# Performance work log

Measured on AMD Instinct MI355X. Metric: run time of the kernel, lower is better.

## Reference

```python
import jax, jax.numpy as jnp
import numpy as np

WS = 7
NHEAD = 8


def setup_inputs() -> dict:
    key = jax.random.key(0)
    k1, k2, k3 = jax.random.split(key, 3)
    B, H, W, D = 32, 56, 56, 256
    x = jax.random.normal(k1, (B, H, W, D), dtype=jnp.float32)
    in_proj_w = jax.random.normal(k2, (3 * D, D), dtype=jnp.float32) * 0.02
    in_proj_b = jnp.zeros((3 * D,), dtype=jnp.float32)
    out_w = jax.random.normal(k3, (D, D), dtype=jnp.float32) * 0.02
    out_b = jnp.zeros((D,), dtype=jnp.float32)
    return {"x": x, "in_proj_w": in_proj_w, "in_proj_b": in_proj_b,
            "out_w": out_w, "out_b": out_b}


def reference(x, in_proj_w, in_proj_b, out_w, out_b):
    B, Hf, Wf, D = x.shape
    ws = WS
    hd = D // NHEAD
    pad_h = (-Hf) % ws
    pad_w = (-Wf) % ws
    xp = jnp.pad(x, ((0, 0), (0, pad_h), (0, pad_w), (0, 0)))
    Hp, Wp = Hf + pad_h, Wf + pad_w
    nh, nw = Hp // ws, Wp // ws
    # partition into windows: [B*nh*nw, ws*ws, D]
    xw = xp.reshape(B, nh, ws, nw, ws, D).transpose(0, 1, 3, 2, 4, 5)
    xw = xw.reshape(B * nh * nw, ws * ws, D)
    N, L = xw.shape[0], ws * ws
    # qkv projection (torch MHA: x @ in_proj_w.T + in_proj_b)
    qkv = jnp.einsum('nld,ed->nle', xw, in_proj_w) + in_proj_b  # [N, L, 3D]
    q, k, v = jnp.split(qkv, 3, axis=-1)
    q = q.reshape(N, L, NHEAD, hd).transpose(0, 2, 1, 3)
    k = k.reshape(N, L, NHEAD, hd).transpose(0, 2, 1, 3)
    v = v.reshape(N, L, NHEAD, hd).transpose(0, 2, 1, 3)
    scale = 1.0 / np.sqrt(hd).astype(np.float32)
    scores = jnp.einsum('nhqd,nhkd->nhqk', q * scale, k)  # [N, H, L, L]
    attn = jax.nn.softmax(scores, axis=-1)
    o = jnp.einsum('nhqk,nhkd->nhqd', attn, v)
    o = o.transpose(0, 2, 1, 3).reshape(N, L, D)
    o = jnp.einsum('nld,ed->nle', o, out_w) + out_b
    # un-window
    o = o.reshape(B, nh, nw, ws, ws, D).transpose(0, 1, 3, 2, 4, 5)
    o = o.reshape(B, Hp, Wp, D)
    return o[:, :Hf, :Wf, :]
```

## Files before the change

### kernel.cpp

```cpp
#include <hip/hip_runtime.h>


using f16   = _Float16;
using f16x4 = __attribute__((ext_vector_type(4))) _Float16;
using f16x8 = __attribute__((ext_vector_type(8))) _Float16;
using f32x4 = __attribute__((ext_vector_type(4))) float;

#define NTOK   100352
#define DMODEL 256
#define QKVN   768
#define QKV_BYTES 154140672ull
#define WQ_HALVES 196608
#define WO_HALVES 65536

typedef const __attribute__((address_space(1))) unsigned int* as1_u32p;
typedef __attribute__((address_space(3))) unsigned int* as3_u32p;

__device__ __forceinline__ void gload16(const void* g, void* l) {
    __builtin_amdgcn_global_load_lds((as1_u32p)g, (as3_u32p)l, 16, 0, 0);
}

__device__ __forceinline__ f16x8 zero8() {
    f16x8 z;
#pragma unroll
    for (int i = 0; i < 8; ++i) z[i] = (f16)0;
    return z;
}

#define XV4   6422528
#define WQV4  49152
#define WOV4  16384
__global__ __launch_bounds__(256) void convert_all(
    const float* __restrict__ X, const float* __restrict__ Wq,
    const float* __restrict__ Wo,
    f16* __restrict__ Xh, f16* __restrict__ Wqh, f16* __restrict__ Woh)
{
    const float scale = 0.17677669529663687f;
    const int total = XV4 + WQV4 + WOV4;
    for (int i = blockIdx.x * blockDim.x + threadIdx.x; i < total;
         i += gridDim.x * blockDim.x) {
        float4 f;
        f16x4 h;
        if (i < XV4) {
            f = reinterpret_cast<const float4*>(X)[i];
            h[0]=(f16)f.x; h[1]=(f16)f.y; h[2]=(f16)f.z; h[3]=(f16)f.w;
            reinterpret_cast<f16x4*>(Xh)[i] = h;
        } else if (i < XV4 + WQV4) {
            int idx = i - XV4;
            int row = idx >> 6;
            float sc = (row < 256) ? scale : 1.0f;
            f = reinterpret_cast<const float4*>(Wq)[idx];
            h[0]=(f16)(f.x*sc); h[1]=(f16)(f.y*sc); h[2]=(f16)(f.z*sc); h[3]=(f16)(f.w*sc);
            reinterpret_cast<f16x4*>(Wqh)[idx] = h;
        } else if (Woh) {
            int idx = i - XV4 - WQV4;
            f = reinterpret_cast<const float4*>(Wo)[idx];
            h[0]=(f16)f.x; h[1]=(f16)f.y; h[2]=(f16)f.z; h[3]=(f16)f.w;
            reinterpret_cast<f16x4*>(Woh)[idx] = h;
        }
    }
}

__global__ __launch_bounds__(256) void qkv_gemm(
    const f16* __restrict__ Xh,
    const f16* __restrict__ Wh,
    const float* __restrict__ bias,
    f16* __restrict__ QKV)
{
    __shared__ f16 As[2][128 * 64];
    __shared__ f16 Bs[2][128 * 64];
    const int tid  = threadIdx.x;
    const int lane = tid & 63;
    const int wave = tid >> 6;
    int wg = blockIdx.x;
    const int cpx = (NTOK / 128) * (QKVN / 128) / 8;
    wg = (wg & 7) * cpx + (wg >> 3);
    const int m0 = (wg / (QKVN / 128)) * 128;
    const int n0 = (wg % (QKVN / 128)) * 128;
    const int wm = (wave >> 1) * 64;
    const int wn = (wave & 1) * 64;
    const int g  = lane >> 4;
    const int lr = lane & 15;

    auto stage = [&](int buf, int k0) {
#pragma unroll
        for (int j = 0; j < 4; ++j) {
            int s   = tid + j * 256;
            int row = s >> 3, sl = s & 7;
            int ss  = sl ^ (row & 7);
            gload16(Xh + (size_t)(m0 + row) * 256 + k0 + ss * 8, &As[buf][s * 8]);
            gload16(Wh + (size_t)(n0 + row) * 256 + k0 + ss * 8, &Bs[buf][s * 8]);
        }
    };

    stage(0, 0);
    __syncthreads();

    f32x4 acc[4][4] = {};
    int buf = 0;
    for (int t = 0; t < 4; ++t) {
        if (t < 3) stage(buf ^ 1, (t + 1) * 64);
#pragma unroll
        for (int ks = 0; ks < 2; ++ks) {
            f16x8 a[4], b[4];
#pragma unroll
            for (int i = 0; i < 4; ++i) {
                int row = wm + i * 16 + lr;
                int c   = ((ks << 2) + g) ^ (row & 7);
                a[i] = *reinterpret_cast<const f16x8*>(&As[buf][row * 64 + c * 8]);
            }
#pragma unroll
            for (int i = 0; i < 4; ++i) {
                int row = wn + i * 16 + lr;
                int c   = ((ks << 2) + g) ^ (row & 7);
                b[i] = *reinterpret_cast<const f16x8*>(&Bs[buf][row * 64 + c * 8]);
            }
#pragma unroll
            for (int mi = 0; mi < 4; ++mi)
#pragma unroll
                for (int ni = 0; ni < 4; ++ni)
                    acc[mi][ni] = __builtin_amdgcn_mfma_f32_16x16x32_f16(a[mi], b[ni], acc[mi][ni], 0, 0, 0);
        }
        __syncthreads();
        buf ^= 1;
    }
    const float scale = 0.17677669529663687f;
#pragma unroll
    for (int ni = 0; ni < 4; ++ni) {
        int n = n0 + wn + ni * 16 + lr;
        float bv = bias[n];
        if (n < 256) bv *= scale;
#pragma unroll
        for (int mi = 0; mi < 4; ++mi)
#pragma unroll
            for (int r = 0; r < 4; ++r) {
                int m = m0 + wm + mi * 16 + g * 4 + r;
                QKV[(size_t)m * QKVN + n] = (f16)(acc[mi][ni][r] + bv);
            }
    }
}

__global__ __launch_bounds__(256) void win_attn(f16* __restrict__ QKV)
{
    __shared__ f16 Vt[4][32][68];
    __shared__ f16 P[4][64][68];
    const int tid  = threadIdx.x;
    const int lane = tid & 63;
    const int w    = tid >> 6;
    const int u    = blockIdx.x * 4 + w;
    const int win = u >> 3, h = u & 7;
    const int b = win >> 6, wh = (win >> 3) & 7, ww = win & 7;
    const int base = (b * 56 + wh * 7) * 56 + ww * 7;
    const int g = lane >> 4, lr = lane & 15;

    auto tok = [&](int row) { int rr = row / 7; return base + rr * 56 + (row - rr * 7); };

    f16x8 qf[4], kf[4];
#pragma unroll
    for (int i = 0; i < 4; ++i) {
        int row = i * 16 + lr;
        if (row < 49) {
            size_t off = (size_t)tok(row) * QKVN + h * 32 + g * 8;
            qf[i] = *reinterpret_cast<const f16x8*>(QKV + off);
            kf[i] = *reinterpret_cast<const f16x8*>(QKV + off + 256);
        } else { qf[i] = zero8(); kf[i] = zero8(); }
    }
    {
        int kk = lane;
        if (kk < 49) {
            size_t off = (size_t)tok(kk) * QKVN + 512 + h * 32;
            f16x8 vv[4];
#pragma unroll
            for (int j = 0; j < 4; ++j)
                vv[j] = *reinterpret_cast<const f16x8*>(QKV + off + j * 8);
#pragma unroll
            for (int j = 0; j < 4; ++j)
#pragma unroll
                for (int d = 0; d < 8; ++d) Vt[w][j * 8 + d][kk] = vv[j][d];
        } else {
#pragma unroll
            for (int d = 0; d < 32; ++d) Vt[w][d][kk] = (f16)0;
        }
    }
    f32x4 s[4][4] = {};
#pragma unroll
    for (int ki = 0; ki < 4; ++ki)
#pragma unroll
        for (int qi = 0; qi < 4; ++qi)
            s[ki][qi] = __builtin_amdgcn_mfma_f32_16x16x32_f16(kf[ki], qf[qi], s[ki][qi], 0, 0, 0);

#pragma unroll
    for (int qi = 0; qi < 4; ++qi) {
        float e[4][4];
        float sum = 0.f;
#pragma unroll
        for (int ki = 0; ki < 4; ++ki)
#pragma unroll
            for (int r = 0; r < 4; ++r)
                e[ki][r] = __expf(s[ki][qi][r]);
#pragma unroll
        for (int ki = 0; ki < 3; ++ki)
#pragma unroll
            for (int r = 0; r < 4; ++r)
                sum += e[ki][r];
        sum += (g == 0) ? e[3][0] : 0.f;
        sum += __shfl_xor(sum, 16, 64);
        sum += __shfl_xor(sum, 32, 64);
        float is = 1.f / sum;
#pragma unroll
        for (int ki = 0; ki < 4; ++ki) {
            f16x4 pw;
            pw[0] = (f16)(e[ki][0] * is);
            pw[1] = (f16)(e[ki][1] * is);
            pw[2] = (f16)(e[ki][2] * is);
            pw[3] = (f16)(e[ki][3] * is);
            *reinterpret_cast<f16x4*>(&P[w][qi * 16 + lr][ki * 16 + g * 4]) = pw;
        }
    }
    __syncthreads();

    f32x4 o[4][2] = {};
#pragma unroll
    for (int ks = 0; ks < 2; ++ks) {
        f16x8 pa[4], vb[2];
#pragma unroll
        for (int mi = 0; mi < 4; ++mi)
            pa[mi] = *reinterpret_cast<const f16x8*>(&P[w][mi * 16 + lr][ks * 32 + g * 8]);
#pragma unroll
        for (int ni = 0; ni < 2; ++ni)
            vb[ni] = *reinterpret_cast<const f16x8*>(&Vt[w][ni * 16 + lr][ks * 32 + g * 8]);
#pragma unroll
        for (int mi = 0; mi < 4; ++mi)
#pragma unroll
            for (int ni = 0; ni < 2; ++ni)
                o[mi][ni] = __builtin_amdgcn_mfma_f32_16x16x32_f16(pa[mi], vb[ni], o[mi][ni], 0, 0, 0);
    }
#pragma unroll
    for (int mi = 0; mi < 4; ++mi)
#pragma unroll
        for (int r = 0; r < 4; ++r) {
            int row = mi * 16 + g * 4 + r;
            if (row < 49) {
                size_t off = (size_t)tok(row) * QKVN + h * 32;
#pragma unroll
                for (int ni = 0; ni < 2; ++ni)
                    QKV[off + ni * 16 + lr] = (f16)o[mi][ni][r];
            }
        }
}

__global__ __launch_bounds__(256) void out_gemm_f16(
    const f16* __restrict__ O,
    const f16* __restrict__ Wh,
    const float* __restrict__ bias,
    float* __restrict__ OUT)
{
    __shared__ f16 As[128 * 64];
    __shared__ f16 Bs[128 * 64];
    const int tid  = threadIdx.x;
    const int lane = tid & 63;
    const int wave = tid >> 6;
    int wg = blockIdx.x;
    const int cpx = (NTOK / 128) * (DMODEL / 128) / 8;
    wg = (wg & 7) * cpx + (wg >> 3);
    const int m0 = (wg / (DMODEL / 128)) * 128;
    const int n0 = (wg % (DMODEL / 128)) * 128;
    const int wm = (wave >> 1) * 64;
    const int wn = (wave & 1) * 64;
    const int g  = lane >> 4;
    const int lr = lane & 15;

    f32x4 acc[4][4] = {};

    for (int k0 = 0; k0 < 256; k0 += 64) {
#pragma unroll
        for (int j = 0; j < 4; ++j) {
            int s   = tid + j * 256;
            int row = s >> 3, sl = s & 7;
            int ss  = sl ^ (row & 7);
            gload16(O + (size_t)(m0 + row) * QKVN + k0 + ss * 8, &As[s * 8]);
            gload16(Wh + (size_t)(n0 + row) * 256 + k0 + ss * 8, &Bs[s * 8]);
        }
        __syncthreads();
#pragma unroll
        for (int ks = 0; ks < 2; ++ks) {
            f16x8 a[4], b[4];
#pragma unroll
            for (int i = 0; i < 4; ++i) {
                int row = wm + i * 16 + lr;
                int c   = ((ks << 2) + g) ^ (row & 7);
                a[i] = *reinterpret_cast<const f16x8*>(&As[row * 64 + c * 8]);
            }
#pragma unroll
            for (int i = 0; i < 4; ++i) {
                int row = wn + i * 16 + lr;
                int c   = ((ks << 2) + g) ^ (row & 7);
                b[i] = *reinterpret_cast<const f16x8*>(&Bs[row * 64 + c * 8]);
            }
#pragma unroll
            for (int mi = 0; mi < 4; ++mi)
#pragma unroll
                for (int ni = 0; ni < 4; ++ni)
                    acc[mi][ni] = __builtin_amdgcn_mfma_f32_16x16x32_f16(a[mi], b[ni], acc[mi][ni], 0, 0, 0);
        }
        __syncthreads();
    }
#pragma unroll
    for (int ni = 0; ni < 4; ++ni) {
        int n = n0 + wn + ni * 16 + lr;
        float bv = bias[n];
#pragma unroll
        for (int mi = 0; mi < 4; ++mi)
#pragma unroll
            for (int r = 0; r < 4; ++r) {
                int m = m0 + wm + mi * 16 + g * 4 + r;
                OUT[(size_t)m * 256 + n] = acc[mi][ni][r] + bv;
            }
    }
}

__global__ __launch_bounds__(256) void out_gemm_cvt(
    const f16* __restrict__ O,
    const float* __restrict__ W,
    const float* __restrict__ bias,
    float* __restrict__ OUT)
{
    __shared__ f16 As[128 * 64];
    __shared__ f16 Bs[128][72];
    const int tid  = threadIdx.x;
    const int lane = tid & 63;
    const int wave = tid >> 6;
    int wg = blockIdx.x;
    const int cpx = (NTOK / 128) * (DMODEL / 128) / 8;
    wg = (wg & 7) * cpx + (wg >> 3);
    const int m0 = (wg / (DMODEL / 128)) * 128;
    const int n0 = (wg % (DMODEL / 128)) * 128;
    const int wm = (wave >> 1) * 64;
    const int wn = (wave & 1) * 64;
    const int g  = lane >> 4;
    const int lr = lane & 15;

    f32x4 acc[4][4] = {};

    for (int k0 = 0; k0 < 256; k0 += 64) {
#pragma unroll
        for (int j = 0; j < 4; ++j) {
            int s   = tid + j * 256;
            int row = s >> 3, sl = s & 7;
            int ss  = sl ^ (row & 7);
            gload16(O + (size_t)(m0 + row) * QKVN + k0 + ss * 8, &As[s * 8]);
        }
#pragma unroll
        for (int j = 0; j < 8; ++j) {
            int v = tid + j * 256;
            int row = v >> 4, cv = v & 15;
            float4 f = *reinterpret_cast<const float4*>(W + (size_t)(n0 + row) * 256 + k0 + cv * 4);
            f16x4 h; h[0]=(f16)f.x; h[1]=(f16)f.y; h[2]=(f16)f.z; h[3]=(f16)f.w;
            *reinterpret_cast<f16x4*>(&Bs[row][cv * 4]) = h;
        }
        __syncthreads();
#pragma unroll
        for (int ks = 0; ks < 2; ++ks) {
            f16x8 a[4], b[4];
#pragma unroll
            for (int i = 0; i < 4; ++i) {
                int row = wm + i * 16 + lr;
                int c   = ((ks << 2) + g) ^ (row & 7);
                a[i] = *reinterpret_cast<const f16x8*>(&As[row * 64 + c * 8]);
            }
#pragma unroll
            for (int i = 0; i < 4; ++i)
                b[i] = *reinterpret_cast<const f16x8*>(&Bs[wn + i * 16 + lr][ks * 32 + g * 8]);
#pragma unroll
            for (int mi = 0; mi < 4; ++mi)
#pragma unroll
                for (int ni = 0; ni < 4; ++ni)
                    acc[mi][ni] = __builtin_amdgcn_mfma_f32_16x16x32_f16(a[mi], b[ni], acc[mi][ni], 0, 0, 0);
        }
        __syncthreads();
    }
#pragma unroll
    for (int ni = 0; ni < 4; ++ni) {
        int n = n0 + wn + ni * 16 + lr;
        float bv = bias[n];
#pragma unroll
        for (int mi = 0; mi < 4; ++mi)
#pragma unroll
            for (int r = 0; r < 4; ++r) {
                int m = m0 + wm + mi * 16 + g * 4 + r;
                OUT[(size_t)m * 256 + n] = acc[mi][ni][r] + bv;
            }
    }
}

extern "C" void kernel_launch(void* const* d_in, const int* in_sizes, int n_in,
                              void* d_out, int out_size, void* d_ws, size_t ws_size,
                              hipStream_t stream) {
    const float* x     = (const float*)d_in[0];
    const float* in_w  = (const float*)d_in[1];
    const float* in_b  = (const float*)d_in[2];
    const float* out_w = (const float*)d_in[3];
    const float* out_b = (const float*)d_in[4];
    float* out = (float*)d_out;
    f16* qkv = (f16*)d_ws;

    f16* xh  = (f16*)d_out;
    f16* wqh = xh + (size_t)NTOK * 256;
    const bool tailok = ws_size >= QKV_BYTES + (size_t)WO_HALVES * 2;
    f16* woh = tailok ? (f16*)((char*)d_ws + QKV_BYTES) : nullptr;

    convert_all<<<2048, 256, 0, stream>>>(x, in_w, out_w, xh, wqh, woh);

    qkv_gemm<<<(NTOK / 128) * (QKVN / 128), 256, 0, stream>>>(xh, wqh, in_b, qkv);

    win_attn<<<4096, 256, 0, stream>>>(qkv);

    if (tailok)
        out_gemm_f16<<<(NTOK / 128) * (DMODEL / 128), 256, 0, stream>>>(qkv, woh, out_b, out);
    else
        out_gemm_cvt<<<(NTOK / 128) * (DMODEL / 128), 256, 0, stream>>>(qkv, out_w, out_b, out);
}
```

Before: 155.9 us.

## Swap MFMA operands for vectorized row-contiguous epilogue stores; single-buffer QKV GEMM

In all three GEMMs the MFMA operands are swapped so each lane's four accumulator values lie along the N dimension. The epilogue can then write f16x4 or float4 vector stores per row with a vector bias load, replacing scattered scalar stores. The QKV GEMM also drops its double-buffered LDS staging for a single buffer with a barrier before compute. That halves its shared memory and may raise occupancy, but global loads no longer overlap with MFMA work inside a block.

```diff
diff --git a/kernel.cpp b/kernel.cpp
--- a/kernel.cpp
+++ b/kernel.cpp
@@ -10,7 +10,6 @@
 #define DMODEL 256
 #define QKVN   768
 #define QKV_BYTES 154140672ull
-#define WQ_HALVES 196608
 #define WO_HALVES 65536
 
 typedef const __attribute__((address_space(1))) unsigned int* as1_u32p;
@@ -67,8 +66,8 @@
     const float* __restrict__ bias,
     f16* __restrict__ QKV)
 {
-    __shared__ f16 As[2][128 * 64];
-    __shared__ f16 Bs[2][128 * 64];
+    __shared__ f16 As[128 * 64];
+    __shared__ f16 Bs[128 * 64];
     const int tid  = threadIdx.x;
     const int lane = tid & 63;
     const int wave = tid >> 6;
@@ -82,24 +81,18 @@
     const int g  = lane >> 4;
     const int lr = lane & 15;
 
-    auto stage = [&](int buf, int k0) {
+    f32x4 acc[4][4] = {};
+
+    for (int k0 = 0; k0 < 256; k0 += 64) {
 #pragma unroll
         for (int j = 0; j < 4; ++j) {
             int s   = tid + j * 256;
             int row = s >> 3, sl = s & 7;
             int ss  = sl ^ (row & 7);
-            gload16(Xh + (size_t)(m0 + row) * 256 + k0 + ss * 8, &As[buf][s * 8]);
-            gload16(Wh + (size_t)(n0 + row) * 256 + k0 + ss * 8, &Bs[buf][s * 8]);
-        }
-    };
-
-    stage(0, 0);
-    __syncthreads();
-
-    f32x4 acc[4][4] = {};
-    int buf = 0;
-    for (int t = 0; t < 4; ++t) {
-        if (t < 3) stage(buf ^ 1, (t + 1) * 64);
+            gload16(Xh + (size_t)(m0 + row) * 256 + k0 + ss * 8, &As[s * 8]);
+            gload16(Wh + (size_t)(n0 + row) * 256 + k0 + ss * 8, &Bs[s * 8]);
+        }
+        __syncthreads();
 #pragma unroll
         for (int ks = 0; ks < 2; ++ks) {
             f16x8 a[4], b[4];
@@ -107,36 +100,38 @@
             for (int i = 0; i < 4; ++i) {
                 int row = wm + i * 16 + lr;
                 int c   = ((ks << 2) + g) ^ (row & 7);
-                a[i] = *reinterpret_cast<const f16x8*>(&As[buf][row * 64 + c * 8]);
+                a[i] = *reinterpret_cast<const f16x8*>(&As[row * 64 + c * 8]);
             }
 #pragma unroll
             for (int i = 0; i < 4; ++i) {
                 int row = wn + i * 16 + lr;
                 int c   = ((ks << 2) + g) ^ (row & 7);
-                b[i] = *reinterpret_cast<const f16x8*>(&Bs[buf][row * 64 + c * 8]);
-            }
-#pragma unroll
-            for (int mi = 0; mi < 4; ++mi)
-#pragma unroll
-                for (int ni = 0; ni < 4; ++ni)
-                    acc[mi][ni] = __builtin_amdgcn_mfma_f32_16x16x32_f16(a[mi], b[ni], acc[mi][ni], 0, 0, 0);
-        }
-        __syncthreads();
-        buf ^= 1;
+                b[i] = *reinterpret_cast<const f16x8*>(&Bs[row * 64 + c * 8]);
+            }
+#pragma unroll
+            for (int ni = 0; ni < 4; ++ni)
+#pragma unroll
+                for (int mi = 0; mi < 4; ++mi)
+                    acc[ni][mi] = __builtin_amdgcn_mfma_f32_16x16x32_f16(b[ni], a[mi], acc[ni][mi], 0, 0, 0);
+        }
+        __syncthreads();
     }
     const float scale = 0.17677669529663687f;
 #pragma unroll
     for (int ni = 0; ni < 4; ++ni) {
-        int n = n0 + wn + ni * 16 + lr;
-        float bv = bias[n];
-        if (n < 256) bv *= scale;
-#pragma unroll
-        for (int mi = 0; mi < 4; ++mi)
-#pragma unroll
-            for (int r = 0; r < 4; ++r) {
-                int m = m0 + wm + mi * 16 + g * 4 + r;
-                QKV[(size_t)m * QKVN + n] = (f16)(acc[mi][ni][r] + bv);
-            }
+        int nb = n0 + wn + ni * 16 + g * 4;
+        float4 b4 = *reinterpret_cast<const float4*>(bias + nb);
+        float sc = (nb < 256) ? scale : 1.0f;
+        float bv[4] = { b4.x * sc, b4.y * sc, b4.z * sc, b4.w * sc };
+#pragma unroll
+        for (int mi = 0; mi < 4; ++mi) {
+            int m = m0 + wm + mi * 16 + lr;
+            f16x4 pw;
+#pragma unroll
+            for (int r = 0; r < 4; ++r)
+                pw[r] = (f16)(acc[ni][mi][r] + bv[r]);
+            *reinterpret_cast<f16x4*>(&QKV[(size_t)m * QKVN + nb]) = pw;
+        }
     }
 }
 
@@ -298,24 +293,27 @@
                 b[i] = *reinterpret_cast<const f16x8*>(&Bs[row * 64 + c * 8]);
             }
 #pragma unroll
-            for (int mi = 0; mi < 4; ++mi)
-#pragma unroll
-                for (int ni = 0; ni < 4; ++ni)
-                    acc[mi][ni] = __builtin_amdgcn_mfma_f32_16x16x32_f16(a[mi], b[ni], acc[mi][ni], 0, 0, 0);
+            for (int ni = 0; ni < 4; ++ni)
+#pragma unroll
+                for (int mi = 0; mi < 4; ++mi)
+                    acc[ni][mi] = __builtin_amdgcn_mfma_f32_16x16x32_f16(b[ni], a[mi], acc[ni][mi], 0, 0, 0);
         }
         __syncthreads();
     }
 #pragma unroll
     for (int ni = 0; ni < 4; ++ni) {
-        int n = n0 + wn + ni * 16 + lr;
-        float bv = bias[n];
-#pragma unroll
-        for (int mi = 0; mi < 4; ++mi)
-#pragma unroll
-            for (int r = 0; r < 4; ++r) {
-                int m = m0 + wm + mi * 16 + g * 4 + r;
-                OUT[(size_t)m * 256 + n] = acc[mi][ni][r] + bv;
-            }
+        int nb = n0 + wn + ni * 16 + g * 4;
+        float4 b4 = *reinterpret_cast<const float4*>(bias + nb);
+#pragma unroll
+        for (int mi = 0; mi < 4; ++mi) {
+            int m = m0 + wm + mi * 16 + lr;
+            float4 ov;
+            ov.x = acc[ni][mi][0] + b4.x;
+            ov.y = acc[ni][mi][1] + b4.y;
+            ov.z = acc[ni][mi][2] + b4.z;
+            ov.w = acc[ni][mi][3] + b4.w;
+            *reinterpret_cast<float4*>(&OUT[(size_t)m * 256 + nb]) = ov;
+        }
     }
 }
 
@@ -372,24 +370,27 @@
             for (int i = 0; i < 4; ++i)
                 b[i] = *reinterpret_cast<const f16x8*>(&Bs[wn + i * 16 + lr][ks * 32 + g * 8]);
 #pragma unroll
-            for (int mi = 0; mi < 4; ++mi)
-#pragma unroll
-                for (int ni = 0; ni < 4; ++ni)
-                    acc[mi][ni] = __builtin_amdgcn_mfma_f32_16x16x32_f16(a[mi], b[ni], acc[mi][ni], 0, 0, 0);
+            for (int ni = 0; ni < 4; ++ni)
+#pragma unroll
+                for (int mi = 0; mi < 4; ++mi)
+                    acc[ni][mi] = __builtin_amdgcn_mfma_f32_16x16x32_f16(b[ni], a[mi], acc[ni][mi], 0, 0, 0);
         }
         __syncthreads();
     }
 #pragma unroll
     for (int ni = 0; ni < 4; ++ni) {
-        int n = n0 + wn + ni * 16 + lr;
-        float bv = bias[n];
-#pragma unroll
-        for (int mi = 0; mi < 4; ++mi)
-#pragma unroll
-            for (int r = 0; r < 4; ++r) {
-                int m = m0 + wm + mi * 16 + g * 4 + r;
-                OUT[(size_t)m * 256 + n] = acc[mi][ni][r] + bv;
-            }
+        int nb = n0 + wn + ni * 16 + g * 4;
+        float4 b4 = *reinterpret_cast<const float4*>(bias + nb);
+#pragma unroll
+        for (int mi = 0; mi < 4; ++mi) {
+            int m = m0 + wm + mi * 16 + lr;
+            float4 ov;
+            ov.x = acc[ni][mi][0] + b4.x;
+            ov.y = acc[ni][mi][1] + b4.y;
+            ov.z = acc[ni][mi][2] + b4.z;
+            ov.w = acc[ni][mi][3] + b4.w;
+            *reinterpret_cast<float4*>(&OUT[(size_t)m * 256 + nb]) = ov;
+        }
     }
 }
 
```

New measurement: 165.4 us. +6.1%, slower.
